# Performance work log

Hardware: AMD Instinct MI355X
Metric: run time of the kernel (lower is better)

## Reference

```python
import jax, jax.numpy as jnp
import numpy as np

UNITS = 1024
BATCH = 32
SEQ = 2048


def setup_inputs() -> dict:
    key = jax.random.key(0)
    ks = jax.random.split(key, 8)
    s = 1.0 / np.sqrt(UNITS)
    return {
        "s_prev": jax.random.normal(ks[0], (BATCH, UNITS), dtype=jnp.float32),
        "hidden_states": jax.random.normal(ks[1], (BATCH, SEQ, UNITS), dtype=jnp.float32),
        "W_w": jax.random.normal(ks[2], (UNITS, UNITS), dtype=jnp.float32) * s,
        "W_b": jnp.zeros((UNITS,), dtype=jnp.float32),
        "U_w": jax.random.normal(ks[3], (UNITS, UNITS), dtype=jnp.float32) * s,
        "U_b": jnp.zeros((UNITS,), dtype=jnp.float32),
        "V_w": jax.random.normal(ks[4], (UNITS, 1), dtype=jnp.float32) * s,
        "V_b": jnp.zeros((1,), dtype=jnp.float32),
    }


def reference(s_prev, hidden_states, W_w, W_b, U_w, U_b, V_w, V_b):
    # decoder: (B, 1, units); encoder: (B, S, units)
    decoder = (s_prev @ W_w + W_b)[:, None, :]
    encoder = jnp.einsum("bsu,uh->bsh", hidden_states, U_w) + U_b
    # scores: (B, S, 1); softmax over sequence axis
    scores = jnp.tanh(decoder + encoder) @ V_w + V_b
    alpha = jax.nn.softmax(scores, axis=1)
    # context: (B, units)
    context = jnp.sum(alpha * hidden_states, axis=1)
    return context, alpha
```

## Files before the change

### kernel.cpp

```cpp
#include <hip/hip_runtime.h>
#include <math.h>

#define U_DIM 1024
#define B_DIM 32
#define S_DIM 2048
#define M_TOT (B_DIM * S_DIM)

typedef _Float16 half8 __attribute__((ext_vector_type(8)));
typedef _Float16 half4v __attribute__((ext_vector_type(4)));
typedef float f32x4 __attribute__((ext_vector_type(4)));

__device__ __forceinline__ void gload_lds16(const void* g, void* l) {
  __builtin_amdgcn_global_load_lds(
      (const __attribute__((address_space(1))) unsigned int*)g,
      (__attribute__((address_space(3))) unsigned int*)l,
      16, 0, 0);
}

__global__ void conv_transpose_uw(const float* __restrict__ Uw,
                                  _Float16* __restrict__ UwT) {
  __shared__ float tile[32][33];
  const int bn = blockIdx.x, bk = blockIdx.y;
  const int c = threadIdx.x & 31, r0 = threadIdx.x >> 5;
#pragma unroll
  for (int it = 0; it < 4; ++it) {
    int r = r0 + it * 8;
    tile[r][c] = Uw[(size_t)(bk * 32 + r) * U_DIM + bn * 32 + c];
  }
  __syncthreads();
#pragma unroll
  for (int it = 0; it < 4; ++it) {
    int r = r0 + it * 8;
    UwT[(size_t)(bn * 32 + r) * U_DIM + bk * 32 + c] = (_Float16)tile[c][r];
  }
}

__launch_bounds__(256)
__global__ void decoder_kernel(const float* __restrict__ sp,
                               const float* __restrict__ Ww,
                               const float* __restrict__ Wb,
                               float* __restrict__ dec) {
  const int h = blockIdx.x * 256 + threadIdx.x;
  const int b = blockIdx.y;
  __shared__ float sprev[256];
  float acc = Wb[h];
  for (int u0 = 0; u0 < U_DIM; u0 += 256) {
    __syncthreads();
    sprev[threadIdx.x] = sp[b * U_DIM + u0 + threadIdx.x];
    __syncthreads();
#pragma unroll 8
    for (int uu = 0; uu < 256; ++uu)
      acc = fmaf(sprev[uu], Ww[(size_t)(u0 + uu) * U_DIM + h], acc);
  }
  dec[b * U_DIM + h] = acc;
}

__launch_bounds__(256)
__global__ void gemm_score_kernel(const float* __restrict__ hs,
                                  const _Float16* __restrict__ UwT,
                                  const float* __restrict__ dec,
                                  const float* __restrict__ Ub,
                                  const float* __restrict__ Vw,
                                  float* __restrict__ score) {
  __shared__ _Float16 As[128 * 32];
  __shared__ _Float16 Bs[128 * 32];

  const int bid = blockIdx.x;
  const int xcd = bid & 7;
  const int i = bid >> 3;
  const int tm = xcd * 64 + (i >> 3);
  const int tn = i & 7;
  const int m0 = tm * 128, n0 = tn * 128;

  const int t = threadIdx.x;
  const int lane = t & 63;
  const int wave = t >> 6;
  const int wr = wave >> 1, wc = wave & 1;

  f32x4 acc[4][4] = {};

  const float* aBase[4];
#pragma unroll
  for (int it = 0; it < 4; ++it) {
    int L = t + 256 * it;
    aBase[it] = hs + (size_t)(m0 + (L >> 3)) * U_DIM + ((L & 7) << 2);
  }
  const _Float16* bBase0 = UwT + (size_t)(n0 + (t >> 2)) * U_DIM + ((t & 3) << 3);
  const _Float16* bBase1 = bBase0 + (size_t)64 * U_DIM;
  _Float16* lB0 = Bs + t * 8;
  _Float16* lB1 = Bs + t * 8 + 2048;
  half4v* lA = (half4v*)As;

  const int lr = lane & 15;
  const int lk = (lane >> 4) << 3;
  const int aoff = (wr * 64 + lr) * 32 + lk;
  const int boff = (wc * 64 + lr) * 32 + lk;

  for (int k0 = 0; k0 < U_DIM; k0 += 32) {
    gload_lds16(bBase0 + k0, lB0);
    gload_lds16(bBase1 + k0, lB1);
#pragma unroll
    for (int it = 0; it < 4; ++it) {
      float4 v = *(const float4*)(aBase[it] + k0);
      half4v h = {(_Float16)v.x, (_Float16)v.y, (_Float16)v.z, (_Float16)v.w};
      lA[t + 256 * it] = h;
    }
    __syncthreads();
    half8 af[4], bf[4];
#pragma unroll
    for (int q = 0; q < 4; ++q) af[q] = *(const half8*)&As[aoff + q * 16 * 32];
#pragma unroll
    for (int q = 0; q < 4; ++q) bf[q] = *(const half8*)&Bs[boff + q * 16 * 32];
#pragma unroll
    for (int a = 0; a < 4; ++a)
#pragma unroll
      for (int bq = 0; bq < 4; ++bq)
        acc[a][bq] = __builtin_amdgcn_mfma_f32_16x16x32_f16(af[a], bf[bq],
                                                            acc[a][bq], 0, 0, 0);
    __syncthreads();
  }

  const int b = m0 >> 11;
  float biasj[4], vwj[4];
#pragma unroll
  for (int j = 0; j < 4; ++j) {
    int n = n0 + wc * 64 + j * 16 + lr;
    biasj[j] = dec[b * U_DIM + n] + Ub[n];
    vwj[j] = Vw[n];
  }
  const int sbase = (m0 & (S_DIM - 1)) + wr * 64 + ((lane >> 4) << 2);
#pragma unroll
  for (int a = 0; a < 4; ++a) {
    float ps0 = 0.f, ps1 = 0.f, ps2 = 0.f, ps3 = 0.f;
#pragma unroll
    for (int j = 0; j < 4; ++j) {
      ps0 += tanhf(acc[a][j][0] + biasj[j]) * vwj[j];
      ps1 += tanhf(acc[a][j][1] + biasj[j]) * vwj[j];
      ps2 += tanhf(acc[a][j][2] + biasj[j]) * vwj[j];
      ps3 += tanhf(acc[a][j][3] + biasj[j]) * vwj[j];
    }
#pragma unroll
    for (int msk = 1; msk < 16; msk <<= 1) {
      ps0 += __shfl_xor(ps0, msk, 64);
      ps1 += __shfl_xor(ps1, msk, 64);
      ps2 += __shfl_xor(ps2, msk, 64);
      ps3 += __shfl_xor(ps3, msk, 64);
    }
    if (lr == 0) {
      float* spp = score + b * S_DIM + sbase + a * 16;
      atomicAdd(spp + 0, ps0);
      atomicAdd(spp + 1, ps1);
      atomicAdd(spp + 2, ps2);
      atomicAdd(spp + 3, ps3);
    }
  }
}

__global__ void softmax_kernel(const float* __restrict__ score,
                               float* __restrict__ alpha) {
  const int b = blockIdx.x;
  const int t = threadIdx.x;
  float vals[8];
  float mx = -1e30f;
#pragma unroll
  for (int k = 0; k < 8; ++k) {
    vals[k] = score[b * S_DIM + t + k * 256];
    mx = fmaxf(mx, vals[k]);
  }
#pragma unroll
  for (int m = 1; m < 64; m <<= 1) mx = fmaxf(mx, __shfl_xor(mx, m, 64));
  __shared__ float smx[4], ssum[4];
  if ((t & 63) == 0) smx[t >> 6] = mx;
  __syncthreads();
  mx = fmaxf(fmaxf(smx[0], smx[1]), fmaxf(smx[2], smx[3]));
  float sum = 0.f;
#pragma unroll
  for (int k = 0; k < 8; ++k) {
    vals[k] = expf(vals[k] - mx);
    sum += vals[k];
  }
#pragma unroll
  for (int m = 1; m < 64; m <<= 1) sum += __shfl_xor(sum, m, 64);
  if ((t & 63) == 0) ssum[t >> 6] = sum;
  __syncthreads();
  sum = ssum[0] + ssum[1] + ssum[2] + ssum[3];
  const float inv = 1.0f / sum;
#pragma unroll
  for (int k = 0; k < 8; ++k)
    alpha[b * S_DIM + t + k * 256] = vals[k] * inv;
}

__launch_bounds__(256)
__global__ void context_kernel(const float* __restrict__ hs,
                               const float* __restrict__ alpha,
                               float* __restrict__ ctx) {
  const int b = blockIdx.y;
  const int sc = blockIdx.x;
  const int t = threadIdx.x;
  __shared__ float al[128];
  if (t < 128) al[t] = alpha[b * S_DIM + sc * 128 + t];
  __syncthreads();
  const float4* hp =
      (const float4*)(hs + ((size_t)b * S_DIM + (size_t)sc * 128) * U_DIM) + t;
  float4 acc = {0.f, 0.f, 0.f, 0.f};
#pragma unroll 4
  for (int ss = 0; ss < 128; ++ss) {
    float a = al[ss];
    float4 h = hp[(size_t)ss * 256];
    acc.x = fmaf(a, h.x, acc.x);
    acc.y = fmaf(a, h.y, acc.y);
    acc.z = fmaf(a, h.z, acc.z);
    acc.w = fmaf(a, h.w, acc.w);
  }
  float* cp = ctx + b * U_DIM + t * 4;
  atomicAdd(cp + 0, acc.x);
  atomicAdd(cp + 1, acc.y);
  atomicAdd(cp + 2, acc.z);
  atomicAdd(cp + 3, acc.w);
}

extern "C" void kernel_launch(void* const* d_in, const int* in_sizes, int n_in,
                              void* d_out, int out_size, void* d_ws,
                              size_t ws_size, hipStream_t stream) {
  const float* s_prev = (const float*)d_in[0];
  const float* hs = (const float*)d_in[1];
  const float* Ww = (const float*)d_in[2];
  const float* Wb = (const float*)d_in[3];
  const float* Uw = (const float*)d_in[4];
  const float* Ub = (const float*)d_in[5];
  const float* Vw = (const float*)d_in[6];

  float* out = (float*)d_out;
  float* ctx = out;
  float* alpha = out + B_DIM * U_DIM;

  char* ws = (char*)d_ws;
  _Float16* UwT = (_Float16*)ws;
  float* dec = (float*)(ws + 2 * 1024 * 1024);
  float* score = (float*)(ws + 2 * 1024 * 1024 + 128 * 1024);

  hipMemsetAsync(score, 0, (size_t)M_TOT * sizeof(float), stream);
  hipMemsetAsync(ctx, 0, (size_t)B_DIM * U_DIM * sizeof(float), stream);

  conv_transpose_uw<<<dim3(32, 32), 256, 0, stream>>>(Uw, UwT);
  decoder_kernel<<<dim3(4, B_DIM), 256, 0, stream>>>(s_prev, Ww, Wb, dec);
  gemm_score_kernel<<<4096, 256, 0, stream>>>(hs, UwT, dec, Ub, Vw, score);
  softmax_kernel<<<B_DIM, 256, 0, stream>>>(score, alpha);
  context_kernel<<<dim3(16, B_DIM), 256, 0, stream>>>(hs, alpha, ctx);
}
```

Baseline: 732.1 us.

## Pre-convert hidden states to fp16 and use pipelined 256x256 MFMA GEMM

```diff
diff --git a/kernel.cpp b/kernel.cpp
--- a/kernel.cpp
+++ b/kernel.cpp
@@ -7,7 +7,6 @@
 #define M_TOT (B_DIM * S_DIM)
 
 typedef _Float16 half8 __attribute__((ext_vector_type(8)));
-typedef _Float16 half4v __attribute__((ext_vector_type(4)));
 typedef float f32x4 __attribute__((ext_vector_type(4)));
 
 __device__ __forceinline__ void gload_lds16(const void* g, void* l) {
@@ -17,6 +16,25 @@
       16, 0, 0);
 }
 
+__device__ __forceinline__ float tanh_fast(float x) {
+  float e = exp2f(x * 2.88539008177792681f);
+  return 1.0f - 2.0f * __builtin_amdgcn_rcpf(e + 1.0f);
+}
+
+__launch_bounds__(256)
+__global__ void convert_hs(const float* __restrict__ in,
+                           _Float16* __restrict__ out, size_t n8) {
+  size_t i = (size_t)blockIdx.x * 256 + threadIdx.x;
+  const size_t stride = (size_t)gridDim.x * 256;
+  for (; i < n8; i += stride) {
+    f32x4 a = ((const f32x4*)in)[2 * i];
+    f32x4 b = ((const f32x4*)in)[2 * i + 1];
+    half8 h = {(_Float16)a.x, (_Float16)a.y, (_Float16)a.z, (_Float16)a.w,
+               (_Float16)b.x, (_Float16)b.y, (_Float16)b.z, (_Float16)b.w};
+    ((half8*)out)[i] = h;
+  }
+}
+
 __global__ void conv_transpose_uw(const float* __restrict__ Uw,
                                   _Float16* __restrict__ UwT) {
   __shared__ float tile[32][33];
@@ -36,123 +54,215 @@
 }
 
 __launch_bounds__(256)
-__global__ void decoder_kernel(const float* __restrict__ sp,
-                               const float* __restrict__ Ww,
-                               const float* __restrict__ Wb,
-                               float* __restrict__ dec) {
-  const int h = blockIdx.x * 256 + threadIdx.x;
-  const int b = blockIdx.y;
-  __shared__ float sprev[256];
-  float acc = Wb[h];
-  for (int u0 = 0; u0 < U_DIM; u0 += 256) {
-    __syncthreads();
-    sprev[threadIdx.x] = sp[b * U_DIM + u0 + threadIdx.x];
-    __syncthreads();
-#pragma unroll 8
-    for (int uu = 0; uu < 256; ++uu)
-      acc = fmaf(sprev[uu], Ww[(size_t)(u0 + uu) * U_DIM + h], acc);
-  }
-  dec[b * U_DIM + h] = acc;
-}
-
-__launch_bounds__(256)
-__global__ void gemm_score_kernel(const float* __restrict__ hs,
-                                  const _Float16* __restrict__ UwT,
-                                  const float* __restrict__ dec,
-                                  const float* __restrict__ Ub,
-                                  const float* __restrict__ Vw,
-                                  float* __restrict__ score) {
-  __shared__ _Float16 As[128 * 32];
-  __shared__ _Float16 Bs[128 * 32];
+__global__ void decoder2(const float* __restrict__ sp,
+                         const float* __restrict__ Ww,
+                         const float* __restrict__ Wb,
+                         float* __restrict__ dec) {
+  const int b = blockIdx.y, u0 = blockIdx.x * 128, t = threadIdx.x;
+  __shared__ float s[128];
+  if (t < 128) s[t] = sp[b * U_DIM + u0 + t];
+  __syncthreads();
+  const f32x4* W4 = (const f32x4*)Ww + (size_t)u0 * 256 + t;
+  f32x4 acc = {0.f, 0.f, 0.f, 0.f};
+#pragma unroll 4
+  for (int uu = 0; uu < 128; ++uu) {
+    f32x4 w = W4[(size_t)uu * 256];
+    float a = s[uu];
+    acc.x = fmaf(a, w.x, acc.x);
+    acc.y = fmaf(a, w.y, acc.y);
+    acc.z = fmaf(a, w.z, acc.z);
+    acc.w = fmaf(a, w.w, acc.w);
+  }
+  if (blockIdx.x == 0) {
+    const f32x4 wb = ((const f32x4*)Wb)[t];
+    acc.x += wb.x; acc.y += wb.y; acc.z += wb.z; acc.w += wb.w;
+  }
+  float* dp = dec + b * U_DIM + t * 4;
+  atomicAdd(dp + 0, acc.x);
+  atomicAdd(dp + 1, acc.y);
+  atomicAdd(dp + 2, acc.z);
+  atomicAdd(dp + 3, acc.w);
+}
+
+__launch_bounds__(512, 2)
+__global__ void gemm_score_8p(const _Float16* __restrict__ Ah,
+                              const _Float16* __restrict__ UwT,
+                              const float* __restrict__ dec,
+                              const float* __restrict__ Ub,
+                              const float* __restrict__ Vw,
+                              float* __restrict__ score) {
+  __shared__ _Float16 As[2][256 * 64];
+  __shared__ _Float16 Bs[2][256 * 64];
 
   const int bid = blockIdx.x;
-  const int xcd = bid & 7;
-  const int i = bid >> 3;
-  const int tm = xcd * 64 + (i >> 3);
-  const int tn = i & 7;
-  const int m0 = tm * 128, n0 = tn * 128;
+  const int lin = (bid & 7) * 128 + (bid >> 3);
+  const int tm = lin >> 2, tn = lin & 3;
+  const int m0 = tm * 256, n0 = tn * 256;
 
   const int t = threadIdx.x;
   const int lane = t & 63;
-  const int wave = t >> 6;
-  const int wr = wave >> 1, wc = wave & 1;
-
-  f32x4 acc[4][4] = {};
-
-  const float* aBase[4];
-#pragma unroll
-  for (int it = 0; it < 4; ++it) {
-    int L = t + 256 * it;
-    aBase[it] = hs + (size_t)(m0 + (L >> 3)) * U_DIM + ((L & 7) << 2);
-  }
-  const _Float16* bBase0 = UwT + (size_t)(n0 + (t >> 2)) * U_DIM + ((t & 3) << 3);
-  const _Float16* bBase1 = bBase0 + (size_t)64 * U_DIM;
-  _Float16* lB0 = Bs + t * 8;
-  _Float16* lB1 = Bs + t * 8 + 2048;
-  half4v* lA = (half4v*)As;
-
-  const int lr = lane & 15;
-  const int lk = (lane >> 4) << 3;
-  const int aoff = (wr * 64 + lr) * 32 + lk;
-  const int boff = (wc * 64 + lr) * 32 + lk;
-
-  for (int k0 = 0; k0 < U_DIM; k0 += 32) {
-    gload_lds16(bBase0 + k0, lB0);
-    gload_lds16(bBase1 + k0, lB1);
-#pragma unroll
-    for (int it = 0; it < 4; ++it) {
-      float4 v = *(const float4*)(aBase[it] + k0);
-      half4v h = {(_Float16)v.x, (_Float16)v.y, (_Float16)v.z, (_Float16)v.w};
-      lA[t + 256 * it] = h;
+  const int w = t >> 6;
+  const int wm = w >> 2, wn = w & 3;
+  const int g = lane >> 4, lr = lane & 15;
+
+  const _Float16* aSrc[4];
+  const _Float16* bSrc[4];
+  int dstOff[4];
+#pragma unroll
+  for (int L = 0; L < 4; ++L) {
+    int c = t + 512 * L;
+    int row = c >> 3;
+    int ls = (c & 7) ^ (row & 7);
+    aSrc[L] = Ah + (size_t)(m0 + row) * U_DIM + ls * 8;
+    bSrc[L] = UwT + (size_t)(n0 + row) * U_DIM + ls * 8;
+    dstOff[L] = c * 8;
+  }
+
+  f32x4 acc[8][4] = {};
+
+  const int aro = (wm * 128 + lr) * 64;
+  const int bro = (wn * 64 + lr) * 64;
+  int slot[2];
+#pragma unroll
+  for (int kk = 0; kk < 2; ++kk) slot[kk] = (((kk << 2) | g) ^ (lr & 7)) * 8;
+
+#pragma unroll
+  for (int L = 0; L < 4; ++L) {
+    gload_lds16(aSrc[L], &As[0][dstOff[L]]);
+    gload_lds16(bSrc[L], &Bs[0][dstOff[L]]);
+  }
+
+  const int NT = U_DIM / 64;
+  for (int kt = 0; kt < NT; ++kt) {
+    const int P = kt & 1;
+    if (kt + 1 < NT) {
+      const int koff = (kt + 1) * 64;
+#pragma unroll
+      for (int L = 0; L < 4; ++L) {
+        gload_lds16(aSrc[L] + koff, &As[P ^ 1][dstOff[L]]);
+        gload_lds16(bSrc[L] + koff, &Bs[P ^ 1][dstOff[L]]);
+      }
+      asm volatile("s_waitcnt vmcnt(8)" ::: "memory");
+    } else {
+      asm volatile("s_waitcnt vmcnt(0)" ::: "memory");
     }
-    __syncthreads();
-    half8 af[4], bf[4];
-#pragma unroll
-    for (int q = 0; q < 4; ++q) af[q] = *(const half8*)&As[aoff + q * 16 * 32];
-#pragma unroll
-    for (int q = 0; q < 4; ++q) bf[q] = *(const half8*)&Bs[boff + q * 16 * 32];
-#pragma unroll
-    for (int a = 0; a < 4; ++a)
-#pragma unroll
-      for (int bq = 0; bq < 4; ++bq)
-        acc[a][bq] = __builtin_amdgcn_mfma_f32_16x16x32_f16(af[a], bf[bq],
-                                                            acc[a][bq], 0, 0, 0);
-    __syncthreads();
-  }
-
+    __builtin_amdgcn_s_barrier();
+    asm volatile("" ::: "memory");
+
+    const _Float16* A_ = As[P];
+    const _Float16* B_ = Bs[P];
+    half8 af[4][2], bf[2][2];
+
+#pragma unroll
+    for (int i = 0; i < 4; ++i)
+#pragma unroll
+      for (int kk = 0; kk < 2; ++kk)
+        af[i][kk] = *(const half8*)&A_[aro + i * 1024 + slot[kk]];
+#pragma unroll
+    for (int j = 0; j < 2; ++j)
+#pragma unroll
+      for (int kk = 0; kk < 2; ++kk)
+        bf[j][kk] = *(const half8*)&B_[bro + j * 1024 + slot[kk]];
+    __builtin_amdgcn_s_setprio(1);
+#pragma unroll
+    for (int i = 0; i < 4; ++i)
+#pragma unroll
+      for (int j = 0; j < 2; ++j)
+#pragma unroll
+        for (int kk = 0; kk < 2; ++kk)
+          acc[i][j] = __builtin_amdgcn_mfma_f32_16x16x32_f16(
+              af[i][kk], bf[j][kk], acc[i][j], 0, 0, 0);
+    __builtin_amdgcn_s_setprio(0);
+    __builtin_amdgcn_s_barrier();
+    asm volatile("" ::: "memory");
+
+#pragma unroll
+    for (int j = 0; j < 2; ++j)
+#pragma unroll
+      for (int kk = 0; kk < 2; ++kk)
+        bf[j][kk] = *(const half8*)&B_[bro + (2 + j) * 1024 + slot[kk]];
+    __builtin_amdgcn_s_setprio(1);
+#pragma unroll
+    for (int i = 0; i < 4; ++i)
+#pragma unroll
+      for (int j = 0; j < 2; ++j)
+#pragma unroll
+        for (int kk = 0; kk < 2; ++kk)
+          acc[i][2 + j] = __builtin_amdgcn_mfma_f32_16x16x32_f16(
+              af[i][kk], bf[j][kk], acc[i][2 + j], 0, 0, 0);
+    __builtin_amdgcn_s_setprio(0);
+    __builtin_amdgcn_s_barrier();
+    asm volatile("" ::: "memory");
+
+#pragma unroll
+    for (int i = 0; i < 4; ++i)
+#pragma unroll
+      for (int kk = 0; kk < 2; ++kk)
+        af[i][kk] = *(const half8*)&A_[aro + 4096 + i * 1024 + slot[kk]];
+    __builtin_amdgcn_s_setprio(1);
+#pragma unroll
+    for (int i = 0; i < 4; ++i)
+#pragma unroll
+      for (int j = 0; j < 2; ++j)
+#pragma unroll
+        for (int kk = 0; kk < 2; ++kk)
+          acc[4 + i][2 + j] = __builtin_amdgcn_mfma_f32_16x16x32_f16(
+              af[i][kk], bf[j][kk], acc[4 + i][2 + j], 0, 0, 0);
+    __builtin_amdgcn_s_setprio(0);
+    __builtin_amdgcn_s_barrier();
+    asm volatile("" ::: "memory");
+
+#pragma unroll
+    for (int j = 0; j < 2; ++j)
+#pragma unroll
+      for (int kk = 0; kk < 2; ++kk)
+        bf[j][kk] = *(const half8*)&B_[bro + j * 1024 + slot[kk]];
+    __builtin_amdgcn_s_setprio(1);
+#pragma unroll
+    for (int i = 0; i < 4; ++i)
+#pragma unroll
+      for (int j = 0; j < 2; ++j)
+#pragma unroll
+        for (int kk = 0; kk < 2; ++kk)
+          acc[4 + i][j] = __builtin_amdgcn_mfma_f32_16x16x32_f16(
+              af[i][kk], bf[j][kk], acc[4 + i][j], 0, 0, 0);
+    __builtin_amdgcn_s_setprio(0);
+    __builtin_amdgcn_s_barrier();
+    asm volatile("" ::: "memory");
+  }
+
+  __syncthreads();
+
+  float* red = (float*)&As[0][0];
   const int b = m0 >> 11;
-  float biasj[4], vwj[4];
+  float biasv[4], vwv[4];
 #pragma unroll
   for (int j = 0; j < 4; ++j) {
-    int n = n0 + wc * 64 + j * 16 + lr;
-    biasj[j] = dec[b * U_DIM + n] + Ub[n];
-    vwj[j] = Vw[n];
-  }
-  const int sbase = (m0 & (S_DIM - 1)) + wr * 64 + ((lane >> 4) << 2);
-#pragma unroll
-  for (int a = 0; a < 4; ++a) {
-    float ps0 = 0.f, ps1 = 0.f, ps2 = 0.f, ps3 = 0.f;
-#pragma unroll
-    for (int j = 0; j < 4; ++j) {
-      ps0 += tanhf(acc[a][j][0] + biasj[j]) * vwj[j];
-      ps1 += tanhf(acc[a][j][1] + biasj[j]) * vwj[j];
-      ps2 += tanhf(acc[a][j][2] + biasj[j]) * vwj[j];
-      ps3 += tanhf(acc[a][j][3] + biasj[j]) * vwj[j];
+    int n = n0 + wn * 64 + j * 16 + lr;
+    biasv[j] = dec[b * U_DIM + n] + Ub[n];
+    vwv[j] = Vw[n];
+  }
+#pragma unroll
+  for (int mi = 0; mi < 8; ++mi)
+#pragma unroll
+    for (int r = 0; r < 4; ++r) {
+      float s = 0.f;
+#pragma unroll
+      for (int j = 0; j < 4; ++j)
+        s += tanh_fast(acc[mi][j][r] + biasv[j]) * vwv[j];
+      int rl = wm * 128 + mi * 16 + g * 4 + r;
+      red[rl * 64 + wn * 16 + lr] = s;
     }
-#pragma unroll
-    for (int msk = 1; msk < 16; msk <<= 1) {
-      ps0 += __shfl_xor(ps0, msk, 64);
-      ps1 += __shfl_xor(ps1, msk, 64);
-      ps2 += __shfl_xor(ps2, msk, 64);
-      ps3 += __shfl_xor(ps3, msk, 64);
+  __syncthreads();
+  if (t < 256) {
+    float sum = 0.f;
+    const f32x4* rp = (const f32x4*)&red[t * 64];
+#pragma unroll
+    for (int k = 0; k < 16; ++k) {
+      f32x4 v = rp[(k + t) & 15];
+      sum += v.x + v.y + v.z + v.w;
     }
-    if (lr == 0) {
-      float* spp = score + b * S_DIM + sbase + a * 16;
-      atomicAdd(spp + 0, ps0);
-      atomicAdd(spp + 1, ps1);
-      atomicAdd(spp + 2, ps2);
-      atomicAdd(spp + 3, ps3);
-    }
+    atomicAdd(score + b * S_DIM + (m0 & (S_DIM - 1)) + t, sum);
   }
 }
 
@@ -191,32 +301,36 @@
 }
 
 __launch_bounds__(256)
-__global__ void context_kernel(const float* __restrict__ hs,
-                               const float* __restrict__ alpha,
-                               float* __restrict__ ctx) {
-  const int b = blockIdx.y;
-  const int sc = blockIdx.x;
-  const int t = threadIdx.x;
-  __shared__ float al[128];
-  if (t < 128) al[t] = alpha[b * S_DIM + sc * 128 + t];
-  __syncthreads();
-  const float4* hp =
-      (const float4*)(hs + ((size_t)b * S_DIM + (size_t)sc * 128) * U_DIM) + t;
-  float4 acc = {0.f, 0.f, 0.f, 0.f};
+__global__ void context_h(const _Float16* __restrict__ hsH,
+                          const float* __restrict__ alpha,
+                          float* __restrict__ ctx) {
+  const int b = blockIdx.y, sc = blockIdx.x, t = threadIdx.x;
+  __shared__ float al[64];
+  __shared__ float red[128][8];
+  if (t < 64) al[t] = alpha[b * S_DIM + sc * 64 + t];
+  __syncthreads();
+  const int hc = t & 127;
+  const int p = t >> 7;
+  const half8* hp =
+      (const half8*)(hsH + ((size_t)b * S_DIM + sc * 64 + p) * U_DIM) + hc;
+  float a8[8] = {};
 #pragma unroll 4
-  for (int ss = 0; ss < 128; ++ss) {
-    float a = al[ss];
-    float4 h = hp[(size_t)ss * 256];
-    acc.x = fmaf(a, h.x, acc.x);
-    acc.y = fmaf(a, h.y, acc.y);
-    acc.z = fmaf(a, h.z, acc.z);
-    acc.w = fmaf(a, h.w, acc.w);
-  }
-  float* cp = ctx + b * U_DIM + t * 4;
-  atomicAdd(cp + 0, acc.x);
-  atomicAdd(cp + 1, acc.y);
-  atomicAdd(cp + 2, acc.z);
-  atomicAdd(cp + 3, acc.w);
+  for (int i = 0; i < 32; ++i) {
+    float a = al[2 * i + p];
+    half8 h = hp[(size_t)i * 256];
+#pragma unroll
+    for (int j = 0; j < 8; ++j) a8[j] = fmaf(a, (float)h[j], a8[j]);
+  }
+  if (p == 1) {
+#pragma unroll
+    for (int j = 0; j < 8; ++j) red[hc][j] = a8[j];
+  }
+  __syncthreads();
+  if (p == 0) {
+    float* cp = ctx + b * U_DIM + hc * 8;
+#pragma unroll
+    for (int j = 0; j < 8; ++j) atomicAdd(cp + j, a8[j] + red[hc][j]);
+  }
 }
 
 extern "C" void kernel_launch(void* const* d_in, const int* in_sizes, int n_in,
@@ -235,16 +349,20 @@
   float* alpha = out + B_DIM * U_DIM;
 
   char* ws = (char*)d_ws;
-  _Float16* UwT = (_Float16*)ws;
-  float* dec = (float*)(ws + 2 * 1024 * 1024);
-  float* score = (float*)(ws + 2 * 1024 * 1024 + 128 * 1024);
-
+  _Float16* hsH = (_Float16*)ws;
+  char* base = ws + (size_t)M_TOT * U_DIM * sizeof(_Float16);
+  _Float16* UwT = (_Float16*)base;
+  float* dec = (float*)(base + 2 * 1024 * 1024);
+  float* score = (float*)(base + 2 * 1024 * 1024 + 128 * 1024);
+
+  hipMemsetAsync(dec, 0, (size_t)B_DIM * U_DIM * sizeof(float), stream);
   hipMemsetAsync(score, 0, (size_t)M_TOT * sizeof(float), stream);
   hipMemsetAsync(ctx, 0, (size_t)B_DIM * U_DIM * sizeof(float), stream);
 
   conv_transpose_uw<<<dim3(32, 32), 256, 0, stream>>>(Uw, UwT);
-  decoder_kernel<<<dim3(4, B_DIM), 256, 0, stream>>>(s_prev, Ww, Wb, dec);
-  gemm_score_kernel<<<4096, 256, 0, stream>>>(hs, UwT, dec, Ub, Vw, score);
+  decoder2<<<dim3(8, B_DIM), 256, 0, stream>>>(s_prev, Ww, Wb, dec);
+  convert_hs<<<4096, 256, 0, stream>>>(hs, hsH, (size_t)M_TOT * U_DIM / 8);
+  gemm_score_8p<<<1024, 512, 0, stream>>>(hsH, UwT, dec, Ub, Vw, score);
   softmax_kernel<<<B_DIM, 256, 0, stream>>>(score, alpha);
-  context_kernel<<<dim3(16, B_DIM), 256, 0, stream>>>(hs, alpha, ctx);
-}
+  context_h<<<dim3(32, B_DIM), 256, 0, stream>>>(hsH, alpha, ctx);
+}
```

Result: faster. 642.6 us (-12.2%).
